# Kernel tuning notes

Hardware: AMD Instinct MI355X
Metric: run time of the kernel (lower is better)

Reference implementation:

```python
import jax, jax.numpy as jnp
import numpy as np

B, S, D, H, KD = 4, 2048, 640, 10, 64


def setup_inputs() -> dict:
    key = jax.random.key(0)
    k0, k1, k2, k3, k4 = jax.random.split(key, 5)
    x = jax.random.normal(k0, (B, S, D), dtype=jnp.float32)
    # per-head projection weights, stacked over heads: [H, D, KD]
    Wq = jax.random.normal(k1, (H, D, KD), dtype=jnp.float32) * 0.05
    Wk = jax.random.normal(k2, (H, D, KD), dtype=jnp.float32) * 0.05
    Wv = jax.random.normal(k3, (H, D, KD), dtype=jnp.float32) * 0.05
    # output projection: [H*KD, D]
    Wo = jax.random.normal(k4, (H * KD, D), dtype=jnp.float32) * 0.05
    return {"x": x, "Wq": Wq, "Wk": Wk, "Wv": Wv, "Wo": Wo}


def reference(x, Wq, Wk, Wv, Wo):
    # Batched equivalent of the per-head Python loop:
    # each head computes q=x@Wq_h, k=x@Wk_h, v=x@Wv_h, softmax(q k^T / sqrt(KD)) @ v
    q = jnp.einsum("bsd,hdk->bhsk", x, Wq)
    k = jnp.einsum("bsd,hdk->bhsk", x, Wk)
    v = jnp.einsum("bsd,hdk->bhsk", x, Wv)
    scale = 1.0 / jnp.sqrt(jnp.asarray(KD, x.dtype))
    scores = jnp.einsum("bhsk,bhtk->bhst", q, k) * scale  # [B,H,S,S]
    attn = jax.nn.softmax(scores, axis=-1)
    z = jnp.einsum("bhst,bhtk->bhsk", attn, v)  # [B,H,S,KD]
    # concat heads along last axis (head 0 first, matching the loop order)
    z = z.transpose(0, 2, 1, 3).reshape(x.shape[0], x.shape[1], H * KD)
    return jnp.einsum("bsf,fd->bsd", z, Wo)
```

## Files before the change

kernel.cpp:

```cpp
#include <hip/hip_runtime.h>
#include <hip/hip_bf16.h>

#define B_  4
#define S_  2048
#define D_  640
#define H_  10
#define KD_ 64

typedef __attribute__((ext_vector_type(8))) short  short8;
typedef __attribute__((ext_vector_type(4))) short  short4v;
typedef __attribute__((ext_vector_type(4))) float  floatx4;
typedef __attribute__((ext_vector_type(2))) unsigned int uint2v;

static __device__ __forceinline__ short f2bf_fast(float f) {
    unsigned int u = __float_as_uint(f);
    u += 0x7fffu + ((u >> 16) & 1u);
    return (short)(u >> 16);
}
static __device__ __forceinline__ unsigned int pack2bf(float a, float b) {
    union { __hip_bfloat162 h; unsigned int u; } c;
    c.h = __float22bfloat162_rn(float2{a, b});
    return c.u;
}

static __device__ __forceinline__ void gload_lds16(const void* gp, void* lp) {
    __builtin_amdgcn_global_load_lds(
        (const __attribute__((address_space(1))) unsigned int*)gp,
        (__attribute__((address_space(3))) unsigned int*)lp, 16, 0, 0);
}

__global__ __launch_bounds__(256) void prep(
        const float* __restrict__ x,
        const float* __restrict__ Wq, const float* __restrict__ Wk,
        const float* __restrict__ Wv, const float* __restrict__ Wo,
        short* __restrict__ xb, short* __restrict__ BigT,
        short* __restrict__ WoT) {
    __shared__ float tile[32][33];
    int bid = blockIdx.x;
    if (bid < 5120) {
        int idx = (bid * 256 + threadIdx.x) * 4;
        float4 v = *(const float4*)(x + idx);
        uint2v o;
        o[0] = pack2bf(v.x, v.y);
        o[1] = pack2bf(v.z, v.w);
        *(uint2v*)(xb + idx) = o;
    } else if (bid < 6320) {
        int flat = bid - 5120;
        int bz = flat / 40, rem = flat % 40;
        int by = rem >> 1, bxx = rem & 1;
        int w = bz / 10, h = bz % 10;
        const float* W = ((w == 0) ? Wq : (w == 1) ? Wk : Wv) + h * 640 * 64;
        short* out = BigT + (w * 640 + h * 64) * 640;
        int c0 = bxx * 32;
        int r0 = by * 32;
        int tx = threadIdx.x & 31, ty = threadIdx.x >> 5;
        #pragma unroll
        for (int k = 0; k < 4; ++k)
            tile[ty + 8 * k][tx] = W[(r0 + ty + 8 * k) * 64 + c0 + tx];
        __syncthreads();
        #pragma unroll
        for (int k = 0; k < 4; ++k)
            out[(c0 + ty + 8 * k) * 640 + r0 + tx] = f2bf_fast(tile[tx][ty + 8 * k]);
    } else {
        int flat = bid - 6320;
        int c0 = (flat % 20) * 32;
        int r0 = (flat / 20) * 32;
        int tx = threadIdx.x & 31, ty = threadIdx.x >> 5;
        #pragma unroll
        for (int k = 0; k < 4; ++k)
            tile[ty + 8 * k][tx] = Wo[(r0 + ty + 8 * k) * 640 + c0 + tx];
        __syncthreads();
        #pragma unroll
        for (int k = 0; k < 4; ++k)
            WoT[(c0 + ty + 8 * k) * 640 + r0 + tx] = f2bf_fast(tile[tx][ty + 8 * k]);
    }
}


__global__ __launch_bounds__(256) void qkv_gemm(
        const short* __restrict__ X, const short* __restrict__ BigT,
        short* __restrict__ qb, short* __restrict__ kb, short* __restrict__ vtb) {
    __shared__ __align__(16) short Ab[2][128][32];
    __shared__ __align__(16) short Bb[2][128][32];

    int wave = threadIdx.x >> 6;
    int lane = threadIdx.x & 63;
    int lq = lane & 15, quad = lane >> 4;
    int wm = (wave & 1) * 64, wn = (wave >> 1) * 64;

    int lin = blockIdx.y * 64 + blockIdx.x;
    int tm = ((lin & 7) * 8 + ((lin >> 3) & 7)) * 128;
    int tn = (lin >> 6) * 128;

    int srow = lane >> 2;
    int schunk = (lane & 3) ^ ((lane >> 3) & 3);
    const short* Asrc0 = X    + (tm + wave * 32 + srow) * 640 + schunk * 8;
    const short* Bsrc0 = BigT + (tn + wave * 32 + srow) * 640 + schunk * 8;
    const short* Asrc1 = Asrc0 + 16 * 640;
    const short* Bsrc1 = Bsrc0 + 16 * 640;

    floatx4 acc[4][4];
    for (int a = 0; a < 4; ++a)
        for (int n = 0; n < 4; ++n)
            acc[a][n] = (floatx4){0.f, 0.f, 0.f, 0.f};

    int rsw = (lq >> 1) & 3;

    gload_lds16(Asrc0, &Ab[0][wave * 32][0]);
    gload_lds16(Asrc1, &Ab[0][wave * 32 + 16][0]);
    gload_lds16(Bsrc0, &Bb[0][wave * 32][0]);
    gload_lds16(Bsrc1, &Bb[0][wave * 32 + 16][0]);

    int p = 0;
    bool isV = (tn >= 1280);

    for (int k0 = 0; k0 < 640; k0 += 32) {
        __syncthreads();
        if (k0 + 32 < 640) {
            int pn = p ^ 1;
            gload_lds16(Asrc0 + k0 + 32, &Ab[pn][wave * 32][0]);
            gload_lds16(Asrc1 + k0 + 32, &Ab[pn][wave * 32 + 16][0]);
            gload_lds16(Bsrc0 + k0 + 32, &Bb[pn][wave * 32][0]);
            gload_lds16(Bsrc1 + k0 + 32, &Bb[pn][wave * 32 + 16][0]);
        }

        short8 af[4], bf[4];
        #pragma unroll
        for (int t = 0; t < 4; ++t) {
            af[t] = *(const short8*)(&Ab[p][wm + t * 16 + lq][(quad ^ rsw) * 8]);
            bf[t] = *(const short8*)(&Bb[p][wn + t * 16 + lq][(quad ^ rsw) * 8]);
        }
        if (!isV) {
            #pragma unroll
            for (int mt = 0; mt < 4; ++mt)
                #pragma unroll
                for (int nt = 0; nt < 4; ++nt)
                    acc[mt][nt] = __builtin_amdgcn_mfma_f32_16x16x32_bf16(
                        bf[nt], af[mt], acc[mt][nt], 0, 0, 0);
        } else {
            #pragma unroll
            for (int mt = 0; mt < 4; ++mt)
                #pragma unroll
                for (int nt = 0; nt < 4; ++nt)
                    acc[mt][nt] = __builtin_amdgcn_mfma_f32_16x16x32_bf16(
                        af[mt], bf[nt], acc[mt][nt], 0, 0, 0);
        }
        p ^= 1;
    }

    if (!isV) {
        const float qscale = 0.18033688011112042f;
        short* dst = (tn < 640) ? qb : kb;
        float scale = (tn < 640) ? qscale : 1.0f;
        #pragma unroll
        for (int nt = 0; nt < 4; ++nt) {
            int rem = (tn + wn + nt * 16) % 640;
            int hh = rem / 64;
            int kd0 = (rem % 64) + quad * 4;
            #pragma unroll
            for (int mt = 0; mt < 4; ++mt) {
                int m = tm + wm + mt * 16 + lq;
                int b = m >> 11, s = m & 2047;
                uint2v w;
                w[0] = pack2bf(acc[mt][nt][0] * scale, acc[mt][nt][1] * scale);
                w[1] = pack2bf(acc[mt][nt][2] * scale, acc[mt][nt][3] * scale);
                *(uint2v*)(dst + (((b * H_ + hh) * S_ + s) * KD_ + kd0)) = w;
            }
        }
    } else {
        #pragma unroll
        for (int nt = 0; nt < 4; ++nt) {
            int rem = (tn + wn + nt * 16) - 1280;
            int hh = rem / 64;
            int kd = (rem % 64) + lq;
            #pragma unroll
            for (int mt = 0; mt < 4; ++mt) {
                int s = tm + wm + mt * 16 + quad * 4;
                int b = s >> 11, s0 = s & 2047;
                uint2v w;
                w[0] = pack2bf(acc[mt][nt][0], acc[mt][nt][1]);
                w[1] = pack2bf(acc[mt][nt][2], acc[mt][nt][3]);
                *(uint2v*)(vtb + (((b * H_ + hh) * KD_ + kd) * (long)S_ + s0)) = w;
            }
        }
    }
}

__global__ __launch_bounds__(256, 3) void attn(
        const short* __restrict__ qb, const short* __restrict__ kbuf,
        const short* __restrict__ vtb, short* __restrict__ zb) {
    __shared__ __align__(16) short Kbuf[3][64][64];
    __shared__ __align__(16) short Vbuf[3][64][64];

    int wave = threadIdx.x >> 6;
    int lane = threadIdx.x & 63;
    int lq = lane & 15, quad = lane >> 4;

    int bx = blockIdx.x;
    int xcd = bx & 7, slot = bx >> 3;
    int bh = xcd * 5 + (slot >> 4);
    int qt = slot & 15;
    int b = bh / 10, h = bh % 10;
    int q0 = qt * 128;

    const short* qp = qb + (b * H_ + h) * S_ * KD_;
    const short* kp = kbuf + (b * H_ + h) * S_ * KD_;
    const short* vp = vtb + (b * H_ + h) * KD_ * S_;

    int r8 = lane >> 3;
    int g  = (lane & 7) ^ r8;
    const short* kg0 = kp + (wave * 16 + r8) * 64 + g * 8;
    const short* kg1 = kp + (wave * 16 + 8 + r8) * 64 + g * 8;
    const short* vg0 = vp + (wave * 16 + r8) * (long)S_ + g * 8;
    const short* vg1 = vp + (wave * 16 + 8 + r8) * (long)S_ + g * 8;

    short8 qA0, qA1, qB0, qB1;
    {
        int rowA = q0 + wave * 32 + lq;
        qA0 = *(const short8*)(qp + rowA * 64 + quad * 8);
        qA1 = *(const short8*)(qp + rowA * 64 + 32 + quad * 8);
        qB0 = *(const short8*)(qp + (rowA + 16) * 64 + quad * 8);
        qB1 = *(const short8*)(qp + (rowA + 16) * 64 + 32 + quad * 8);
    }

    short8 ones;
    #pragma unroll
    for (int i = 0; i < 8; ++i) ones[i] = (short)0x3F80;

    floatx4 OA[4], OB[4];
    for (int n = 0; n < 4; ++n) {
        OA[n] = (floatx4){0.f, 0.f, 0.f, 0.f};
        OB[n] = (floatx4){0.f, 0.f, 0.f, 0.f};
    }
    floatx4 lsvA = (floatx4){0.f, 0.f, 0.f, 0.f};
    floatx4 lsvB = (floatx4){0.f, 0.f, 0.f, 0.f};

    int sw = lq & 7;

    #define STAGE_KV(tt, bi) do { \
        gload_lds16(kg0 + (tt) * 4096, &Kbuf[bi][wave * 16][0]); \
        gload_lds16(kg1 + (tt) * 4096, &Kbuf[bi][wave * 16 + 8][0]); \
        gload_lds16(vg0 + (tt) * 64,   &Vbuf[bi][wave * 16][0]); \
        gload_lds16(vg1 + (tt) * 64,   &Vbuf[bi][wave * 16 + 8][0]); \
    } while (0)

    auto compute_tile = [&](int bi) {
        const short* Kb = &Kbuf[bi][0][0];
        const short* Vb = &Vbuf[bi][0][0];

        floatx4 sTA[4], sTB[4];
        __builtin_amdgcn_s_setprio(1);
        #pragma unroll
        for (int kblk = 0; kblk < 4; ++kblk) {
            const short* krow = Kb + (kblk * 16 + lq) * 64;
            short8 bk0 = *(const short8*)(krow + (quad ^ sw) * 8);
            short8 bk1 = *(const short8*)(krow + ((quad + 4) ^ sw) * 8);
            floatx4 zA = (floatx4){0.f, 0.f, 0.f, 0.f};
            zA = __builtin_amdgcn_mfma_f32_16x16x32_bf16(bk0, qA0, zA, 0, 0, 0);
            sTA[kblk] = __builtin_amdgcn_mfma_f32_16x16x32_bf16(bk1, qA1, zA, 0, 0, 0);
            floatx4 zB = (floatx4){0.f, 0.f, 0.f, 0.f};
            zB = __builtin_amdgcn_mfma_f32_16x16x32_bf16(bk0, qB0, zB, 0, 0, 0);
            sTB[kblk] = __builtin_amdgcn_mfma_f32_16x16x32_bf16(bk1, qB1, zB, 0, 0, 0);
        }
        __builtin_amdgcn_s_setprio(0);

        #pragma unroll
        for (int ts = 0; ts < 2; ++ts) {
            int ka = ts * 2, kc = ts * 2 + 1;
            unsigned int a00 = pack2bf(__builtin_amdgcn_exp2f(sTA[ka][0]),
                                       __builtin_amdgcn_exp2f(sTA[ka][1]));
            unsigned int a01 = pack2bf(__builtin_amdgcn_exp2f(sTA[ka][2]),
                                       __builtin_amdgcn_exp2f(sTA[ka][3]));
            unsigned int a10 = pack2bf(__builtin_amdgcn_exp2f(sTA[kc][0]),
                                       __builtin_amdgcn_exp2f(sTA[kc][1]));
            unsigned int a11 = pack2bf(__builtin_amdgcn_exp2f(sTA[kc][2]),
                                       __builtin_amdgcn_exp2f(sTA[kc][3]));
            uint2v sa0 = __builtin_amdgcn_permlane32_swap(a00, a10, false, false);
            uint2v sa1 = __builtin_amdgcn_permlane32_swap(a01, a11, false, false);
            uint2v wa02 = __builtin_amdgcn_permlane16_swap(sa0[0], sa0[1], false, false);
            uint2v wa13 = __builtin_amdgcn_permlane16_swap(sa1[0], sa1[1], false, false);
            union { unsigned int u[4]; short8 s8; } pfa;
            pfa.u[0] = wa02[0];
            pfa.u[1] = wa13[0];
            pfa.u[2] = wa02[1];
            pfa.u[3] = wa13[1];
            short8 pfA = pfa.s8;
            unsigned int b00 = pack2bf(__builtin_amdgcn_exp2f(sTB[ka][0]),
                                       __builtin_amdgcn_exp2f(sTB[ka][1]));
            unsigned int b01 = pack2bf(__builtin_amdgcn_exp2f(sTB[ka][2]),
                                       __builtin_amdgcn_exp2f(sTB[ka][3]));
            unsigned int b10 = pack2bf(__builtin_amdgcn_exp2f(sTB[kc][0]),
                                       __builtin_amdgcn_exp2f(sTB[kc][1]));
            unsigned int b11 = pack2bf(__builtin_amdgcn_exp2f(sTB[kc][2]),
                                       __builtin_amdgcn_exp2f(sTB[kc][3]));
            uint2v sb0 = __builtin_amdgcn_permlane32_swap(b00, b10, false, false);
            uint2v sb1 = __builtin_amdgcn_permlane32_swap(b01, b11, false, false);
            uint2v wb02 = __builtin_amdgcn_permlane16_swap(sb0[0], sb0[1], false, false);
            uint2v wb13 = __builtin_amdgcn_permlane16_swap(sb1[0], sb1[1], false, false);
            union { unsigned int u[4]; short8 s8; } pfb;
            pfb.u[0] = wb02[0];
            pfb.u[1] = wb13[0];
            pfb.u[2] = wb02[1];
            pfb.u[3] = wb13[1];
            short8 pfB = pfb.s8;

            __builtin_amdgcn_s_setprio(1);
            lsvA = __builtin_amdgcn_mfma_f32_16x16x32_bf16(ones, pfA, lsvA, 0, 0, 0);
            lsvB = __builtin_amdgcn_mfma_f32_16x16x32_bf16(ones, pfB, lsvB, 0, 0, 0);
            #pragma unroll
            for (int db = 0; db < 4; ++db) {
                const short* vrow = Vb + (db * 16 + lq) * 64;
                short8 bv = *(const short8*)(vrow + ((ts * 4 + quad) ^ sw) * 8);
                OA[db] = __builtin_amdgcn_mfma_f32_16x16x32_bf16(bv, pfA, OA[db], 0, 0, 0);
                OB[db] = __builtin_amdgcn_mfma_f32_16x16x32_bf16(bv, pfB, OB[db], 0, 0, 0);
            }
            __builtin_amdgcn_s_setprio(0);
        }
    };

    STAGE_KV(0, 0);
    STAGE_KV(1, 1);

    int bi = 0;
    for (int t = 0; t < 30; ++t) {
        asm volatile("s_waitcnt vmcnt(4)\n\ts_barrier" ::: "memory");
        int bn = bi + 2;
        if (bn >= 3) bn -= 3;
        STAGE_KV(t + 2, bn);
        compute_tile(bi);
        ++bi;
        if (bi == 3) bi = 0;
    }
    asm volatile("s_waitcnt vmcnt(4)\n\ts_barrier" ::: "memory");
    compute_tile(bi);
    ++bi;
    if (bi == 3) bi = 0;
    asm volatile("s_waitcnt vmcnt(0)\n\ts_barrier" ::: "memory");
    compute_tile(bi);

    #undef STAGE_KV

    float invA = 1.0f / lsvA[0];
    float invB = 1.0f / lsvB[0];

    int sA = q0 + wave * 32 + lq;
    int sB = sA + 16;
    short* zrA = zb + (b * S_ + sA) * 640 + h * 64;
    short* zrB = zb + (b * S_ + sB) * 640 + h * 64;
    #pragma unroll
    for (int db = 0; db < 4; ++db) {
        uint2v za, zv;
        za[0] = pack2bf(OA[db][0] * invA, OA[db][1] * invA);
        za[1] = pack2bf(OA[db][2] * invA, OA[db][3] * invA);
        *(uint2v*)(zrA + db * 16 + quad * 4) = za;
        zv[0] = pack2bf(OB[db][0] * invB, OB[db][1] * invB);
        zv[1] = pack2bf(OB[db][2] * invB, OB[db][3] * invB);
        *(uint2v*)(zrB + db * 16 + quad * 4) = zv;
    }
}

__global__ __launch_bounds__(256) void out_gemm(
        const short* __restrict__ Z, const short* __restrict__ WoT,
        float* __restrict__ out) {
    __shared__ __align__(16) short Ab[2][128][32];
    __shared__ __align__(16) short Bb[2][64][32];

    int wave = threadIdx.x >> 6;
    int lane = threadIdx.x & 63;
    int lq = lane & 15, quad = lane >> 4;
    int wm = (wave & 1) * 64;
    int wn = (wave >> 1) * 32;

    int lin = blockIdx.y * 64 + blockIdx.x;
    int tm = ((lin & 7) * 8 + ((lin >> 3) & 7)) * 128;
    int tn = (lin >> 6) * 64;

    int srow = lane >> 2;
    int schunk = (lane & 3) ^ ((lane >> 3) & 3);
    const short* Asrc0 = Z   + (tm + wave * 32 + srow) * 640 + schunk * 8;
    const short* Asrc1 = Asrc0 + 16 * 640;
    const short* Bsrc0 = WoT + (tn + wave * 16 + srow) * 640 + schunk * 8;

    floatx4 acc[4][2];
    for (int a = 0; a < 4; ++a)
        for (int n = 0; n < 2; ++n)
            acc[a][n] = (floatx4){0.f, 0.f, 0.f, 0.f};

    int rsw = (lq >> 1) & 3;

    gload_lds16(Asrc0, &Ab[0][wave * 32][0]);
    gload_lds16(Asrc1, &Ab[0][wave * 32 + 16][0]);
    gload_lds16(Bsrc0, &Bb[0][wave * 16][0]);

    int p = 0;
    for (int k0 = 0; k0 < 640; k0 += 32) {
        __syncthreads();
        if (k0 + 32 < 640) {
            int pn = p ^ 1;
            gload_lds16(Asrc0 + k0 + 32, &Ab[pn][wave * 32][0]);
            gload_lds16(Asrc1 + k0 + 32, &Ab[pn][wave * 32 + 16][0]);
            gload_lds16(Bsrc0 + k0 + 32, &Bb[pn][wave * 16][0]);
        }

        short8 af[4], bf[2];
        #pragma unroll
        for (int t = 0; t < 4; ++t)
            af[t] = *(const short8*)(&Ab[p][wm + t * 16 + lq][(quad ^ rsw) * 8]);
        #pragma unroll
        for (int u = 0; u < 2; ++u)
            bf[u] = *(const short8*)(&Bb[p][wn + u * 16 + lq][(quad ^ rsw) * 8]);
        #pragma unroll
        for (int mt = 0; mt < 4; ++mt)
            #pragma unroll
            for (int nt = 0; nt < 2; ++nt)
                acc[mt][nt] = __builtin_amdgcn_mfma_f32_16x16x32_bf16(
                    bf[nt], af[mt], acc[mt][nt], 0, 0, 0);
        p ^= 1;
    }

    #pragma unroll
    for (int mt = 0; mt < 4; ++mt) {
        int m = tm + wm + mt * 16 + lq;
        #pragma unroll
        for (int nt = 0; nt < 2; ++nt) {
            int n0 = tn + wn + nt * 16 + quad * 4;
            float4 v;
            v.x = acc[mt][nt][0];
            v.y = acc[mt][nt][1];
            v.z = acc[mt][nt][2];
            v.w = acc[mt][nt][3];
            *(float4*)(out + m * 640 + n0) = v;
        }
    }
}

extern "C" void kernel_launch(void* const* d_in, const int* in_sizes, int n_in,
                              void* d_out, int out_size, void* d_ws, size_t ws_size,
                              hipStream_t stream) {
    const float* x  = (const float*)d_in[0];
    const float* Wq = (const float*)d_in[1];
    const float* Wk = (const float*)d_in[2];
    const float* Wv = (const float*)d_in[3];
    const float* Wo = (const float*)d_in[4];
    float* out = (float*)d_out;

    char* ws = (char*)d_ws;
    short* BigT = (short*)(ws);
    short* WoT  = (short*)(ws + 2457600);
    short* xb   = (short*)(ws + 3276800);
    short* qb   = (short*)(ws + 13762560);
    short* kb   = (short*)(ws + 24248320);
    short* vtb  = (short*)(ws + 34734080);
    short* zb   = (short*)(ws + 45219840);

    prep<<<dim3(6720), dim3(256), 0, stream>>>(x, Wq, Wk, Wv, Wo, xb, BigT, WoT);
    qkv_gemm<<<dim3(64, 15), dim3(256), 0, stream>>>(xb, BigT, qb, kb, vtb);
    attn<<<dim3(640), dim3(256), 0, stream>>>(qb, kb, vtb, zb);
    out_gemm<<<dim3(64, 10), dim3(256), 0, stream>>>(zb, WoT, out);
}
```

Before: 193.5 us.

## Software-pipeline QK^T of the next tile with softmax·V of the current tile

```diff
diff --git a/kernel.cpp b/kernel.cpp
--- a/kernel.cpp
+++ b/kernel.cpp
@@ -237,108 +237,121 @@
 
     int sw = lq & 7;
 
-    #define STAGE_KV(tt, bi) do { \
+    #define STAGE_K(tt, bi) do { \
         gload_lds16(kg0 + (tt) * 4096, &Kbuf[bi][wave * 16][0]); \
         gload_lds16(kg1 + (tt) * 4096, &Kbuf[bi][wave * 16 + 8][0]); \
+    } while (0)
+    #define STAGE_V(tt, bi) do { \
         gload_lds16(vg0 + (tt) * 64,   &Vbuf[bi][wave * 16][0]); \
         gload_lds16(vg1 + (tt) * 64,   &Vbuf[bi][wave * 16 + 8][0]); \
     } while (0)
 
-    auto compute_tile = [&](int bi) {
-        const short* Kb = &Kbuf[bi][0][0];
-        const short* Vb = &Vbuf[bi][0][0];
-
-        floatx4 sTA[4], sTB[4];
-        __builtin_amdgcn_s_setprio(1);
-        #pragma unroll
-        for (int kblk = 0; kblk < 4; ++kblk) {
-            const short* krow = Kb + (kblk * 16 + lq) * 64;
-            short8 bk0 = *(const short8*)(krow + (quad ^ sw) * 8);
-            short8 bk1 = *(const short8*)(krow + ((quad + 4) ^ sw) * 8);
-            floatx4 zA = (floatx4){0.f, 0.f, 0.f, 0.f};
-            zA = __builtin_amdgcn_mfma_f32_16x16x32_bf16(bk0, qA0, zA, 0, 0, 0);
-            sTA[kblk] = __builtin_amdgcn_mfma_f32_16x16x32_bf16(bk1, qA1, zA, 0, 0, 0);
-            floatx4 zB = (floatx4){0.f, 0.f, 0.f, 0.f};
-            zB = __builtin_amdgcn_mfma_f32_16x16x32_bf16(bk0, qB0, zB, 0, 0, 0);
-            sTB[kblk] = __builtin_amdgcn_mfma_f32_16x16x32_bf16(bk1, qB1, zB, 0, 0, 0);
-        }
-        __builtin_amdgcn_s_setprio(0);
-
-        #pragma unroll
-        for (int ts = 0; ts < 2; ++ts) {
-            int ka = ts * 2, kc = ts * 2 + 1;
-            unsigned int a00 = pack2bf(__builtin_amdgcn_exp2f(sTA[ka][0]),
-                                       __builtin_amdgcn_exp2f(sTA[ka][1]));
-            unsigned int a01 = pack2bf(__builtin_amdgcn_exp2f(sTA[ka][2]),
-                                       __builtin_amdgcn_exp2f(sTA[ka][3]));
-            unsigned int a10 = pack2bf(__builtin_amdgcn_exp2f(sTA[kc][0]),
-                                       __builtin_amdgcn_exp2f(sTA[kc][1]));
-            unsigned int a11 = pack2bf(__builtin_amdgcn_exp2f(sTA[kc][2]),
-                                       __builtin_amdgcn_exp2f(sTA[kc][3]));
-            uint2v sa0 = __builtin_amdgcn_permlane32_swap(a00, a10, false, false);
-            uint2v sa1 = __builtin_amdgcn_permlane32_swap(a01, a11, false, false);
-            uint2v wa02 = __builtin_amdgcn_permlane16_swap(sa0[0], sa0[1], false, false);
-            uint2v wa13 = __builtin_amdgcn_permlane16_swap(sa1[0], sa1[1], false, false);
-            union { unsigned int u[4]; short8 s8; } pfa;
-            pfa.u[0] = wa02[0];
-            pfa.u[1] = wa13[0];
-            pfa.u[2] = wa02[1];
-            pfa.u[3] = wa13[1];
-            short8 pfA = pfa.s8;
-            unsigned int b00 = pack2bf(__builtin_amdgcn_exp2f(sTB[ka][0]),
-                                       __builtin_amdgcn_exp2f(sTB[ka][1]));
-            unsigned int b01 = pack2bf(__builtin_amdgcn_exp2f(sTB[ka][2]),
-                                       __builtin_amdgcn_exp2f(sTB[ka][3]));
-            unsigned int b10 = pack2bf(__builtin_amdgcn_exp2f(sTB[kc][0]),
-                                       __builtin_amdgcn_exp2f(sTB[kc][1]));
-            unsigned int b11 = pack2bf(__builtin_amdgcn_exp2f(sTB[kc][2]),
-                                       __builtin_amdgcn_exp2f(sTB[kc][3]));
-            uint2v sb0 = __builtin_amdgcn_permlane32_swap(b00, b10, false, false);
-            uint2v sb1 = __builtin_amdgcn_permlane32_swap(b01, b11, false, false);
-            uint2v wb02 = __builtin_amdgcn_permlane16_swap(sb0[0], sb0[1], false, false);
-            uint2v wb13 = __builtin_amdgcn_permlane16_swap(sb1[0], sb1[1], false, false);
-            union { unsigned int u[4]; short8 s8; } pfb;
-            pfb.u[0] = wb02[0];
-            pfb.u[1] = wb13[0];
-            pfb.u[2] = wb02[1];
-            pfb.u[3] = wb13[1];
-            short8 pfB = pfb.s8;
-
-            __builtin_amdgcn_s_setprio(1);
-            lsvA = __builtin_amdgcn_mfma_f32_16x16x32_bf16(ones, pfA, lsvA, 0, 0, 0);
-            lsvB = __builtin_amdgcn_mfma_f32_16x16x32_bf16(ones, pfB, lsvB, 0, 0, 0);
-            #pragma unroll
-            for (int db = 0; db < 4; ++db) {
-                const short* vrow = Vb + (db * 16 + lq) * 64;
-                short8 bv = *(const short8*)(vrow + ((ts * 4 + quad) ^ sw) * 8);
-                OA[db] = __builtin_amdgcn_mfma_f32_16x16x32_bf16(bv, pfA, OA[db], 0, 0, 0);
-                OB[db] = __builtin_amdgcn_mfma_f32_16x16x32_bf16(bv, pfB, OB[db], 0, 0, 0);
-            }
-            __builtin_amdgcn_s_setprio(0);
-        }
-    };
-
-    STAGE_KV(0, 0);
-    STAGE_KV(1, 1);
-
-    int bi = 0;
-    for (int t = 0; t < 30; ++t) {
-        asm volatile("s_waitcnt vmcnt(4)\n\ts_barrier" ::: "memory");
-        int bn = bi + 2;
-        if (bn >= 3) bn -= 3;
-        STAGE_KV(t + 2, bn);
-        compute_tile(bi);
-        ++bi;
-        if (bi == 3) bi = 0;
-    }
-    asm volatile("s_waitcnt vmcnt(4)\n\ts_barrier" ::: "memory");
-    compute_tile(bi);
-    ++bi;
-    if (bi == 3) bi = 0;
+    #define QKT(Kbase, dstA, dstB) do { \
+        const short* Kb_ = (Kbase); \
+        __builtin_amdgcn_s_setprio(1); \
+        _Pragma("unroll") \
+        for (int kblk = 0; kblk < 4; ++kblk) { \
+            const short* krow = Kb_ + (kblk * 16 + lq) * 64; \
+            short8 bk0 = *(const short8*)(krow + (quad ^ sw) * 8); \
+            short8 bk1 = *(const short8*)(krow + ((quad + 4) ^ sw) * 8); \
+            floatx4 zA = (floatx4){0.f, 0.f, 0.f, 0.f}; \
+            zA = __builtin_amdgcn_mfma_f32_16x16x32_bf16(bk0, qA0, zA, 0, 0, 0); \
+            dstA[kblk] = __builtin_amdgcn_mfma_f32_16x16x32_bf16(bk1, qA1, zA, 0, 0, 0); \
+            floatx4 zB = (floatx4){0.f, 0.f, 0.f, 0.f}; \
+            zB = __builtin_amdgcn_mfma_f32_16x16x32_bf16(bk0, qB0, zB, 0, 0, 0); \
+            dstB[kblk] = __builtin_amdgcn_mfma_f32_16x16x32_bf16(bk1, qB1, zB, 0, 0, 0); \
+        } \
+        __builtin_amdgcn_s_setprio(0); \
+    } while (0)
+
+    #define SMPV(srcA, srcB, Vbase) do { \
+        const short* Vb_ = (Vbase); \
+        _Pragma("unroll") \
+        for (int ts = 0; ts < 2; ++ts) { \
+            int ka = ts * 2, kc = ts * 2 + 1; \
+            unsigned int a00 = pack2bf(__builtin_amdgcn_exp2f(srcA[ka][0]), \
+                                       __builtin_amdgcn_exp2f(srcA[ka][1])); \
+            unsigned int a01 = pack2bf(__builtin_amdgcn_exp2f(srcA[ka][2]), \
+                                       __builtin_amdgcn_exp2f(srcA[ka][3])); \
+            unsigned int a10 = pack2bf(__builtin_amdgcn_exp2f(srcA[kc][0]), \
+                                       __builtin_amdgcn_exp2f(srcA[kc][1])); \
+            unsigned int a11 = pack2bf(__builtin_amdgcn_exp2f(srcA[kc][2]), \
+                                       __builtin_amdgcn_exp2f(srcA[kc][3])); \
+            uint2v sa0 = __builtin_amdgcn_permlane32_swap(a00, a10, false, false); \
+            uint2v sa1 = __builtin_amdgcn_permlane32_swap(a01, a11, false, false); \
+            uint2v wa02 = __builtin_amdgcn_permlane16_swap(sa0[0], sa0[1], false, false); \
+            uint2v wa13 = __builtin_amdgcn_permlane16_swap(sa1[0], sa1[1], false, false); \
+            union { unsigned int u[4]; short8 s8; } pfa; \
+            pfa.u[0] = wa02[0]; pfa.u[1] = wa13[0]; \
+            pfa.u[2] = wa02[1]; pfa.u[3] = wa13[1]; \
+            short8 pfA = pfa.s8; \
+            unsigned int b00 = pack2bf(__builtin_amdgcn_exp2f(srcB[ka][0]), \
+                                       __builtin_amdgcn_exp2f(srcB[ka][1])); \
+            unsigned int b01 = pack2bf(__builtin_amdgcn_exp2f(srcB[ka][2]), \
+                                       __builtin_amdgcn_exp2f(srcB[ka][3])); \
+            unsigned int b10 = pack2bf(__builtin_amdgcn_exp2f(srcB[kc][0]), \
+                                       __builtin_amdgcn_exp2f(srcB[kc][1])); \
+            unsigned int b11 = pack2bf(__builtin_amdgcn_exp2f(srcB[kc][2]), \
+                                       __builtin_amdgcn_exp2f(srcB[kc][3])); \
+            uint2v sb0 = __builtin_amdgcn_permlane32_swap(b00, b10, false, false); \
+            uint2v sb1 = __builtin_amdgcn_permlane32_swap(b01, b11, false, false); \
+            uint2v wb02 = __builtin_amdgcn_permlane16_swap(sb0[0], sb0[1], false, false); \
+            uint2v wb13 = __builtin_amdgcn_permlane16_swap(sb1[0], sb1[1], false, false); \
+            union { unsigned int u[4]; short8 s8; } pfb; \
+            pfb.u[0] = wb02[0]; pfb.u[1] = wb13[0]; \
+            pfb.u[2] = wb02[1]; pfb.u[3] = wb13[1]; \
+            short8 pfB = pfb.s8; \
+            __builtin_amdgcn_s_setprio(1); \
+            lsvA = __builtin_amdgcn_mfma_f32_16x16x32_bf16(ones, pfA, lsvA, 0, 0, 0); \
+            lsvB = __builtin_amdgcn_mfma_f32_16x16x32_bf16(ones, pfB, lsvB, 0, 0, 0); \
+            _Pragma("unroll") \
+            for (int db = 0; db < 4; ++db) { \
+                const short* vrow = Vb_ + (db * 16 + lq) * 64; \
+                short8 bv = *(const short8*)(vrow + ((ts * 4 + quad) ^ sw) * 8); \
+                OA[db] = __builtin_amdgcn_mfma_f32_16x16x32_bf16(bv, pfA, OA[db], 0, 0, 0); \
+                OB[db] = __builtin_amdgcn_mfma_f32_16x16x32_bf16(bv, pfB, OB[db], 0, 0, 0); \
+            } \
+            __builtin_amdgcn_s_setprio(0); \
+        } \
+    } while (0)
+
+    floatx4 cA[4], cB[4], nA[4], nB[4];
+
+    STAGE_K(0, 0);
+    STAGE_V(0, 0);
+    STAGE_K(1, 1);
+    STAGE_V(1, 1);
+    STAGE_K(2, 2);
+    asm volatile("s_waitcnt vmcnt(8)\n\ts_barrier" ::: "memory");
+    QKT(&Kbuf[0][0][0], cA, cB);
+
+    for (int t2 = 0; t2 < 30; t2 += 2) {
+        {
+            asm volatile("s_waitcnt vmcnt(4)\n\ts_barrier" ::: "memory");
+            STAGE_V(t2 + 2, (t2 + 2) % 3);
+            STAGE_K(t2 + 3, t2 % 3);
+            QKT(&Kbuf[(t2 + 1) % 3][0][0], nA, nB);
+            SMPV(cA, cB, &Vbuf[t2 % 3][0][0]);
+        }
+        {
+            int t = t2 + 1;
+            asm volatile("s_waitcnt vmcnt(4)\n\ts_barrier" ::: "memory");
+            STAGE_V(t + 2, (t + 2) % 3);
+            if (t <= 28) STAGE_K(t + 3, t % 3);
+            QKT(&Kbuf[(t + 1) % 3][0][0], cA, cB);
+            SMPV(nA, nB, &Vbuf[t % 3][0][0]);
+        }
+    }
+    asm volatile("s_waitcnt vmcnt(2)\n\ts_barrier" ::: "memory");
+    QKT(&Kbuf[1][0][0], nA, nB);
+    SMPV(cA, cB, &Vbuf[0][0][0]);
     asm volatile("s_waitcnt vmcnt(0)\n\ts_barrier" ::: "memory");
-    compute_tile(bi);
-
-    #undef STAGE_KV
+    SMPV(nA, nB, &Vbuf[1][0][0]);
+
+    #undef STAGE_K
+    #undef STAGE_V
+    #undef QKT
+    #undef SMPV
 
     float invA = 1.0f / lsvA[0];
     float invB = 1.0f / lsvB[0];
```

New measurement: 194.5 us. No clear change (+0.5%).

## Split attention keys into two halves with a separate combine kernel

Applied to the files above, without the earlier changes.

```diff
diff --git a/kernel.cpp b/kernel.cpp
--- a/kernel.cpp
+++ b/kernel.cpp
@@ -11,6 +11,7 @@
 typedef __attribute__((ext_vector_type(4))) short  short4v;
 typedef __attribute__((ext_vector_type(4))) float  floatx4;
 typedef __attribute__((ext_vector_type(2))) unsigned int uint2v;
+typedef __attribute__((ext_vector_type(4))) unsigned int uint4v;
 
 static __device__ __forceinline__ short f2bf_fast(float f) {
     unsigned int u = __float_as_uint(f);
@@ -21,6 +22,9 @@
     union { __hip_bfloat162 h; unsigned int u; } c;
     c.h = __float22bfloat162_rn(float2{a, b});
     return c.u;
+}
+static __device__ __forceinline__ float bf2f(short v) {
+    return __uint_as_float(((unsigned int)(unsigned short)v) << 16);
 }
 
 static __device__ __forceinline__ void gload_lds16(const void* gp, void* lp) {
@@ -188,9 +192,10 @@
 
 __global__ __launch_bounds__(256, 3) void attn(
         const short* __restrict__ qb, const short* __restrict__ kbuf,
-        const short* __restrict__ vtb, short* __restrict__ zb) {
-    __shared__ __align__(16) short Kbuf[3][64][64];
-    __shared__ __align__(16) short Vbuf[3][64][64];
+        const short* __restrict__ vtb, short* __restrict__ zp0,
+        short* __restrict__ zp1, float* __restrict__ lsvb) {
+    __shared__ __align__(16) short Kbuf[2][64][64];
+    __shared__ __align__(16) short Vbuf[2][64][64];
 
     int wave = threadIdx.x >> 6;
     int lane = threadIdx.x & 63;
@@ -198,14 +203,16 @@
 
     int bx = blockIdx.x;
     int xcd = bx & 7, slot = bx >> 3;
-    int bh = xcd * 5 + (slot >> 4);
-    int qt = slot & 15;
+    int bh = xcd * 5 + (slot >> 5);
+    int rest = slot & 31;
+    int qt = rest >> 1;
+    int half = rest & 1;
     int b = bh / 10, h = bh % 10;
     int q0 = qt * 128;
 
     const short* qp = qb + (b * H_ + h) * S_ * KD_;
-    const short* kp = kbuf + (b * H_ + h) * S_ * KD_;
-    const short* vp = vtb + (b * H_ + h) * KD_ * S_;
+    const short* kp = kbuf + (b * H_ + h) * S_ * KD_ + half * 1024 * KD_;
+    const short* vp = vtb + (b * H_ + h) * KD_ * S_ + half * 1024;
 
     int r8 = lane >> 3;
     int g  = (lane & 7) ^ r8;
@@ -235,18 +242,27 @@
     floatx4 lsvA = (floatx4){0.f, 0.f, 0.f, 0.f};
     floatx4 lsvB = (floatx4){0.f, 0.f, 0.f, 0.f};
 
+    gload_lds16(kg0, &Kbuf[0][wave * 16][0]);
+    gload_lds16(kg1, &Kbuf[0][wave * 16 + 8][0]);
+    gload_lds16(vg0, &Vbuf[0][wave * 16][0]);
+    gload_lds16(vg1, &Vbuf[0][wave * 16 + 8][0]);
+
+    int p = 0;
     int sw = lq & 7;
 
-    #define STAGE_KV(tt, bi) do { \
-        gload_lds16(kg0 + (tt) * 4096, &Kbuf[bi][wave * 16][0]); \
-        gload_lds16(kg1 + (tt) * 4096, &Kbuf[bi][wave * 16 + 8][0]); \
-        gload_lds16(vg0 + (tt) * 64,   &Vbuf[bi][wave * 16][0]); \
-        gload_lds16(vg1 + (tt) * 64,   &Vbuf[bi][wave * 16 + 8][0]); \
-    } while (0)
-
-    auto compute_tile = [&](int bi) {
-        const short* Kb = &Kbuf[bi][0][0];
-        const short* Vb = &Vbuf[bi][0][0];
+    for (int t0 = 0; t0 < 1024; t0 += 64) {
+        __syncthreads();
+
+        if (t0 + 64 < 1024) {
+            int pn = p ^ 1;
+            gload_lds16(kg0 + (t0 + 64) * 64, &Kbuf[pn][wave * 16][0]);
+            gload_lds16(kg1 + (t0 + 64) * 64, &Kbuf[pn][wave * 16 + 8][0]);
+            gload_lds16(vg0 + (t0 + 64),      &Vbuf[pn][wave * 16][0]);
+            gload_lds16(vg1 + (t0 + 64),      &Vbuf[pn][wave * 16 + 8][0]);
+        }
+
+        const short* Kb = &Kbuf[p][0][0];
+        const short* Vb = &Vbuf[p][0][0];
 
         floatx4 sTA[4], sTB[4];
         __builtin_amdgcn_s_setprio(1);
@@ -316,47 +332,57 @@
             }
             __builtin_amdgcn_s_setprio(0);
         }
-    };
-
-    STAGE_KV(0, 0);
-    STAGE_KV(1, 1);
-
-    int bi = 0;
-    for (int t = 0; t < 30; ++t) {
-        asm volatile("s_waitcnt vmcnt(4)\n\ts_barrier" ::: "memory");
-        int bn = bi + 2;
-        if (bn >= 3) bn -= 3;
-        STAGE_KV(t + 2, bn);
-        compute_tile(bi);
-        ++bi;
-        if (bi == 3) bi = 0;
-    }
-    asm volatile("s_waitcnt vmcnt(4)\n\ts_barrier" ::: "memory");
-    compute_tile(bi);
-    ++bi;
-    if (bi == 3) bi = 0;
-    asm volatile("s_waitcnt vmcnt(0)\n\ts_barrier" ::: "memory");
-    compute_tile(bi);
-
-    #undef STAGE_KV
-
-    float invA = 1.0f / lsvA[0];
-    float invB = 1.0f / lsvB[0];
-
+
+        p ^= 1;
+    }
+
+    short* dst = half ? zp1 : zp0;
     int sA = q0 + wave * 32 + lq;
     int sB = sA + 16;
-    short* zrA = zb + (b * S_ + sA) * 640 + h * 64;
-    short* zrB = zb + (b * S_ + sB) * 640 + h * 64;
+    short* zrA = dst + (b * S_ + sA) * 640 + h * 64;
+    short* zrB = dst + (b * S_ + sB) * 640 + h * 64;
     #pragma unroll
     for (int db = 0; db < 4; ++db) {
         uint2v za, zv;
-        za[0] = pack2bf(OA[db][0] * invA, OA[db][1] * invA);
-        za[1] = pack2bf(OA[db][2] * invA, OA[db][3] * invA);
+        za[0] = pack2bf(OA[db][0], OA[db][1]);
+        za[1] = pack2bf(OA[db][2], OA[db][3]);
         *(uint2v*)(zrA + db * 16 + quad * 4) = za;
-        zv[0] = pack2bf(OB[db][0] * invB, OB[db][1] * invB);
-        zv[1] = pack2bf(OB[db][2] * invB, OB[db][3] * invB);
+        zv[0] = pack2bf(OB[db][0], OB[db][1]);
+        zv[1] = pack2bf(OB[db][2], OB[db][3]);
         *(uint2v*)(zrB + db * 16 + quad * 4) = zv;
     }
+    if (quad == 0) {
+        float* lp = lsvb + half * (B_ * H_ * S_) + (b * H_ + h) * S_;
+        lp[sA] = lsvA[0];
+        lp[sB] = lsvB[0];
+    }
+}
+
+__global__ __launch_bounds__(256) void combine(
+        const short* __restrict__ zp1, const float* __restrict__ lsvb,
+        short* __restrict__ zb) {
+    int idx = blockIdx.x * 256 + threadIdx.x;
+    int row = idx / 80;
+    int col = (idx - row * 80) * 8;
+    int b = row >> 11, s = row & 2047;
+    int h = col >> 6;
+    int li = (b * H_ + h) * S_ + s;
+    float inv = 1.0f / (lsvb[li] + lsvb[B_ * H_ * S_ + li]);
+
+    const short* a0 = zb  + row * 640 + col;
+    const short* a1 = zp1 + row * 640 + col;
+    short8 p0 = *(const short8*)a0;
+    short8 p1 = *(const short8*)a1;
+    float f[8];
+    #pragma unroll
+    for (int i = 0; i < 8; ++i)
+        f[i] = (bf2f(p0[i]) + bf2f(p1[i])) * inv;
+    uint4v o;
+    o[0] = pack2bf(f[0], f[1]);
+    o[1] = pack2bf(f[2], f[3]);
+    o[2] = pack2bf(f[4], f[5]);
+    o[3] = pack2bf(f[6], f[7]);
+    *(uint4v*)(zb + row * 640 + col) = o;
 }
 
 __global__ __launch_bounds__(256) void out_gemm(
@@ -452,9 +478,12 @@
     short* kb   = (short*)(ws + 24248320);
     short* vtb  = (short*)(ws + 34734080);
     short* zb   = (short*)(ws + 45219840);
+    short* zp1  = xb;
+    float* lsvb = (float*)ws;
 
     prep<<<dim3(6720), dim3(256), 0, stream>>>(x, Wq, Wk, Wv, Wo, xb, BigT, WoT);
     qkv_gemm<<<dim3(64, 15), dim3(256), 0, stream>>>(xb, BigT, qb, kb, vtb);
-    attn<<<dim3(640), dim3(256), 0, stream>>>(qb, kb, vtb, zb);
+    attn<<<dim3(1280), dim3(256), 0, stream>>>(qb, kb, vtb, zb, zp1, lsvb);
+    combine<<<dim3(2560), dim3(256), 0, stream>>>(zp1, lsvb, zb);
     out_gemm<<<dim3(64, 10), dim3(256), 0, stream>>>(zb, WoT, out);
 }
```

After: 192.5 us. Within noise of the previous version (-0.5%).
